# Performance work log

Measured on AMD Instinct MI355X. Metric: run time of the kernel, lower is better.

The kernel has to match this reference:

```python
import jax, jax.numpy as jnp
import numpy as np

N_ATOMS = 100000
N_BONDS = 200000
N_MOLS = 4000
ATOMS_PER_MOL = 25
MAX_NB = 6
ATOM_FDIM = 133
BOND_FDIM = 14
HIDDEN = 300
DEPTH = 3


def setup_inputs() -> dict:
    key = jax.random.key(0)
    ks = jax.random.split(key, 8)
    f_atoms = jax.random.normal(ks[0], (N_ATOMS, ATOM_FDIM), dtype=jnp.float32)
    f_bonds = jax.random.normal(ks[1], (N_BONDS, BOND_FDIM), dtype=jnp.float32)
    # incoming-bond lists per atom (irregular gather targets)
    a2b = jax.random.randint(ks[2], (N_ATOMS, MAX_NB), 0, N_BONDS, dtype=jnp.int32)
    # source atom of each directed bond
    b2a = jax.random.randint(ks[3], (N_BONDS,), 0, N_ATOMS, dtype=jnp.int32)
    # reverse bond: directed bonds come in pairs (2i, 2i+1)
    b2revb = (jnp.arange(N_BONDS, dtype=jnp.int32) ^ 1)
    # contiguous [start, size] per molecule
    starts = jnp.arange(N_MOLS, dtype=jnp.int32) * ATOMS_PER_MOL
    sizes = jnp.full((N_MOLS,), ATOMS_PER_MOL, dtype=jnp.int32)
    a_scope = jnp.stack([starts, sizes], axis=1)
    W_i = jax.random.normal(ks[4], (HIDDEN, ATOM_FDIM + BOND_FDIM), dtype=jnp.float32) * 0.05
    W_h = jax.random.normal(ks[5], (HIDDEN, HIDDEN), dtype=jnp.float32) * 0.05
    W_o = jax.random.normal(ks[6], (HIDDEN, ATOM_FDIM + HIDDEN), dtype=jnp.float32) * 0.05
    b_o = jax.random.normal(ks[7], (HIDDEN,), dtype=jnp.float32) * 0.05
    return {"f_atoms": f_atoms, "f_bonds": f_bonds, "a2b": a2b, "b2a": b2a,
            "b2revb": b2revb, "a_scope": a_scope, "W_i": W_i, "W_h": W_h,
            "W_o": W_o, "b_o": b_o}


def reference(f_atoms, f_bonds, a2b, b2a, b2revb, a_scope, W_i, W_h, W_o, b_o):
    # initial directed-bond messages: [f_atoms[src], f_bonds] -> Linear -> ReLU
    input_feats = jnp.concatenate([f_atoms[b2a], f_bonds], axis=1)  # (E, 147)
    message = jax.nn.relu(input_feats @ W_i.T)  # (E, H)
    for _ in range(DEPTH - 1):
        nei_a_message = message[a2b].sum(axis=1)          # (V, H) gather+sum
        nei_message = nei_a_message[b2a] - message[b2revb]  # (E, H)
        message = jax.nn.relu(nei_message @ W_h.T)
    a_message = message[a2b].sum(axis=1)  # (V, H)
    atom_hiddens = jax.nn.relu(jnp.concatenate([f_atoms, a_message], axis=1) @ W_o.T + b_o)
    # vectorized scope mean-pool (scopes are contiguous ranges)
    starts = a_scope[:, 0]
    sizes = a_scope[:, 1]
    seg_ids = jnp.searchsorted(starts, jnp.arange(atom_hiddens.shape[0]), side='right') - 1
    sums = jax.ops.segment_sum(atom_hiddens, seg_ids, num_segments=N_MOLS)
    denom = jnp.maximum(sizes, 1).astype(atom_hiddens.dtype)[:, None]
    mol_vecs = jnp.where((sizes > 0)[:, None], sums / denom, 0.0)
    return mol_vecs
```

## Files before the change

### kernel.cpp

```cpp
#include <hip/hip_runtime.h>
#include <stdint.h>

#define N_ATOMS   100000
#define N_BONDS   200000
#define N_MOLS    4000
#define MAX_NB    6
#define ATOM_FDIM 133
#define BOND_FDIM 14
#define HIDDEN    300
#define NPAD      320

typedef __attribute__((ext_vector_type(8))) short          bf16x8;
typedef __attribute__((ext_vector_type(8))) unsigned short u16x8;
typedef __attribute__((ext_vector_type(4))) float          f32x4;
typedef __attribute__((ext_vector_type(4))) unsigned int   u32x4;

static __device__ __forceinline__ float u2f(unsigned int u) {
  union { unsigned int u; float f; } v; v.u = u; return v.f;
}
static __device__ __forceinline__ unsigned int f2u(float f) {
  union { float f; unsigned int u; } v; v.f = f; return v.u;
}
static __device__ __forceinline__ float bflo(unsigned int u) { return u2f(u << 16); }
static __device__ __forceinline__ float bfhi(unsigned int u) { return u2f(u & 0xffff0000u); }
static __device__ __forceinline__ unsigned short f2bf_rn(float f) {
  unsigned int u = f2u(f);
  return (unsigned short)((u + 0x7fffu + ((u >> 16) & 1u)) >> 16);
}
static __device__ __forceinline__ unsigned int pack_rn(float lo, float hi) {
  return ((unsigned int)f2bf_rn(hi) << 16) | f2bf_rn(lo);
}

__global__ __launch_bounds__(256) void convw_kernel(
    const float* __restrict__ w, unsigned short* __restrict__ o,
    int Ksrc, int seg1, int src2off, int seg2dst, int seg2len, int KP) {
  int total = NPAD * KP;
  for (int idx = blockIdx.x * 256 + threadIdx.x; idx < total; idx += gridDim.x * 256) {
    int n = idx / KP, k = idx - n * KP;
    int src = -1;
    if (k < seg1) src = k;
    else if (k >= seg2dst && k < seg2dst + seg2len) src = src2off + (k - seg2dst);
    float v = (n < HIDDEN && src >= 0) ? w[(size_t)n * Ksrc + src] : 0.f;
    o[idx] = f2bf_rn(v);
  }
}

template<int KP, int SRC, bool RELU, bool BIAS>
__global__ __launch_bounds__(256, 2) void gemm_bp(
    const float* __restrict__ Af, const float* __restrict__ F2,
    const unsigned short* Ab, const unsigned short* __restrict__ Nei,
    const int* __restrict__ gmap, const unsigned short* __restrict__ W,
    const float* __restrict__ bias, unsigned short* out, int M) {
  constexpr int NST = KP / 32;
  __shared__ __align__(16) unsigned short As[NST * 2048];

  const int b0   = blockIdx.x * 64;
  const int tid  = threadIdx.x;
  const int lane = tid & 63;
  const int wave = tid >> 6;
  const int sr   = tid >> 2;
  const int q    = tid & 3;

  int row = b0 + sr;
  if (row >= M) row = M - 1;
  int g = 0;
  if (SRC == 0 || SRC == 3) g = gmap[row];
  const int rev = row ^ 1;
  const int dbase = (sr >> 4) * 512 + (q * 16 + (sr & 15)) * 8;

  auto stage_chunk = [&](int ks) -> u16x8 {
    const int kc = ks * 32 + q * 8;
    u16x8 r;
    if (SRC == 1) {
      r = *(const u16x8*)(Ab + (size_t)row * KP + kc);
    } else if (SRC == 3) {
      u16x8 n8 = *(const u16x8*)(Nei + (size_t)g * NPAD + kc);
      u16x8 z8 = *(const u16x8*)(Ab + (size_t)rev * NPAD + kc);
#pragma unroll
      for (int j = 0; j < 8; j += 2) {
        unsigned int nu = ((const unsigned int*)&n8)[j >> 1];
        unsigned int zu = ((const unsigned int*)&z8)[j >> 1];
        float lo = bflo(nu) - bflo(zu), hi = bfhi(nu) - bfhi(zu);
        lo = lo > 0.f ? lo : 0.f; hi = hi > 0.f ? hi : 0.f;
        ((unsigned int*)&r)[j >> 1] = pack_rn(lo, hi);
      }
    } else if (SRC == 0) {
#pragma unroll
      for (int j = 0; j < 8; j++) {
        int k = kc + j; float v = 0.f;
        if (k < ATOM_FDIM) v = Af[(size_t)g * ATOM_FDIM + k];
        else if (k >= 160 && k < 160 + BOND_FDIM) v = F2[(size_t)row * BOND_FDIM + (k - 160)];
        r[j] = f2bf_rn(v);
      }
    } else {
      if (kc >= 160) {
        r = *(const u16x8*)(Ab + (size_t)row * NPAD + (kc - 160));
      } else {
#pragma unroll
        for (int j = 0; j < 8; j++) {
          int k = kc + j;
          r[j] = (k < ATOM_FDIM) ? f2bf_rn(Af[(size_t)row * ATOM_FDIM + k]) : (unsigned short)0;
        }
      }
    }
    return r;
  };

  constexpr int G = (NST < 5) ? NST : 5;
#pragma unroll
  for (int ks0 = 0; ks0 < NST; ks0 += G) {
    u16x8 vals[G];
#pragma unroll
    for (int j = 0; j < G; j++) { int ks = ks0 + j; if (ks < NST) vals[j] = stage_chunk(ks); }
#pragma unroll
    for (int j = 0; j < G; j++) { int ks = ks0 + j; if (ks < NST) *(u16x8*)&As[ks * 2048 + dbase] = vals[j]; }
  }
  __syncthreads();

  f32x4 acc[4][5];
#pragma unroll
  for (int m = 0; m < 4; m++)
#pragma unroll
    for (int n = 0; n < 5; n++) acc[m][n] = (f32x4){0.f, 0.f, 0.f, 0.f};

  const int nbase = wave * 80;
  const int ar = lane & 15, kq = lane >> 4;
  const unsigned short* Wl = W + (size_t)(nbase + ar) * KP + kq * 8;

  bf16x8 bnxt[5];
#pragma unroll
  for (int nf = 0; nf < 5; nf++) bnxt[nf] = *(const bf16x8*)(Wl + (size_t)nf * 16 * KP);

#pragma unroll
  for (int ks = 0; ks < NST; ks++) {
    bf16x8 bcur[5];
#pragma unroll
    for (int nf = 0; nf < 5; nf++) bcur[nf] = bnxt[nf];
    if (ks + 1 < NST) {
#pragma unroll
      for (int nf = 0; nf < 5; nf++)
        bnxt[nf] = *(const bf16x8*)(Wl + (size_t)nf * 16 * KP + (ks + 1) * 32);
    }
    bf16x8 af[4];
#pragma unroll
    for (int m = 0; m < 4; m++) af[m] = *(const bf16x8*)&As[ks * 2048 + m * 512 + lane * 8];
#pragma unroll
    for (int nf = 0; nf < 5; nf++)
#pragma unroll
      for (int m = 0; m < 4; m++)
        acc[m][nf] = __builtin_amdgcn_mfma_f32_16x16x32_bf16(af[m], bcur[nf], acc[m][nf], 0, 0, 0);
  }

#pragma unroll
  for (int m = 0; m < 4; m++) {
#pragma unroll
    for (int rr = 0; rr < 4; rr++) {
      int orow = b0 + m * 16 + kq * 4 + rr;
      if (orow >= M) continue;
#pragma unroll
      for (int nf = 0; nf < 5; nf++) {
        int ocol = nbase + nf * 16 + ar;
        float v = acc[m][nf][rr];
        if (BIAS) v += (ocol < HIDDEN) ? bias[ocol] : 0.f;
        if (RELU) v = v > 0.f ? v : 0.f;
        out[(size_t)orow * NPAD + ocol] = f2bf_rn(v);
      }
    }
  }
}

__global__ __launch_bounds__(256) void agg_kernel(
    const unsigned short* __restrict__ src, const int* __restrict__ a2b,
    unsigned short* __restrict__ dst) {
  const int TPA = NPAD / 16;
  int idx = blockIdx.x * 256 + threadIdx.x;
  if (idx >= N_ATOMS * TPA) return;
  int a  = idx / TPA;
  int kc = (idx - a * TPA) * 16;
  int bidx[MAX_NB];
#pragma unroll
  for (int j = 0; j < MAX_NB; j++) bidx[j] = a2b[a * MAX_NB + j];
  float slo[8], shi[8];
#pragma unroll
  for (int t = 0; t < 8; t++) { slo[t] = 0.f; shi[t] = 0.f; }
#pragma unroll
  for (int j = 0; j < MAX_NB; j++) {
    const u32x4* p = (const u32x4*)(src + (size_t)bidx[j] * NPAD + kc);
    u32x4 v0 = p[0], v1 = p[1];
#pragma unroll
    for (int t = 0; t < 4; t++) {
      slo[t]     += bflo(v0[t]); shi[t]     += bfhi(v0[t]);
      slo[4 + t] += bflo(v1[t]); shi[4 + t] += bfhi(v1[t]);
    }
  }
  u32x4 o0, o1;
#pragma unroll
  for (int t = 0; t < 4; t++) { o0[t] = pack_rn(slo[t], shi[t]); o1[t] = pack_rn(slo[4 + t], shi[4 + t]); }
  u32x4* qp = (u32x4*)(dst + (size_t)a * NPAD + kc);
  qp[0] = o0; qp[1] = o1;
}

__global__ __launch_bounds__(256) void combineH_kernel(
    const unsigned short* __restrict__ neiZ, const unsigned short* Zh,
    const int* __restrict__ b2a, unsigned short* msg) {
  const int TPB = NPAD / 16;
  const int NPAIR = N_BONDS / 2;
  int idx = blockIdx.x * 256 + threadIdx.x;
  if (idx >= NPAIR * TPB) return;
  int p  = idx / TPB;
  int kc = (idx - p * TPB) * 16;
  int b0i = 2 * p, b1i = 2 * p + 1;
  int g0 = b2a[b0i], g1 = b2a[b1i];
  const u32x4* pn0 = (const u32x4*)(neiZ + (size_t)g0 * NPAD + kc);
  const u32x4* pn1 = (const u32x4*)(neiZ + (size_t)g1 * NPAD + kc);
  const u32x4* pz0 = (const u32x4*)(Zh + (size_t)b1i * NPAD + kc);
  const u32x4* pz1 = (const u32x4*)(Zh + (size_t)b0i * NPAD + kc);
  u32x4 n00 = pn0[0], n01 = pn0[1], n10 = pn1[0], n11 = pn1[1];
  u32x4 z00 = pz0[0], z01 = pz0[1], z10 = pz1[0], z11 = pz1[1];
  u32x4 o00, o01, o10, o11;
#pragma unroll
  for (int t = 0; t < 4; t++) {
    float a, c;
    a = bflo(n00[t]) - bflo(z00[t]); c = bfhi(n00[t]) - bfhi(z00[t]);
    o00[t] = pack_rn(a > 0.f ? a : 0.f, c > 0.f ? c : 0.f);
    a = bflo(n01[t]) - bflo(z01[t]); c = bfhi(n01[t]) - bfhi(z01[t]);
    o01[t] = pack_rn(a > 0.f ? a : 0.f, c > 0.f ? c : 0.f);
    a = bflo(n10[t]) - bflo(z10[t]); c = bfhi(n10[t]) - bfhi(z10[t]);
    o10[t] = pack_rn(a > 0.f ? a : 0.f, c > 0.f ? c : 0.f);
    a = bflo(n11[t]) - bflo(z11[t]); c = bfhi(n11[t]) - bfhi(z11[t]);
    o11[t] = pack_rn(a > 0.f ? a : 0.f, c > 0.f ? c : 0.f);
  }
  u32x4* q0 = (u32x4*)(msg + (size_t)b0i * NPAD + kc);
  u32x4* q1 = (u32x4*)(msg + (size_t)b1i * NPAD + kc);
  q0[0] = o00; q0[1] = o01; q1[0] = o10; q1[1] = o11;
}

__global__ __launch_bounds__(256) void readout_kernel(
    const unsigned short* __restrict__ hidden, const int* __restrict__ a_scope,
    float* __restrict__ out) {
  const int TPM = NPAD / 8;
  int idx = blockIdx.x * 256 + threadIdx.x;
  if (idx >= N_MOLS * TPM) return;
  int m = idx / TPM;
  int c = (idx - m * TPM) * 8;
  int start = a_scope[m * 2], size = a_scope[m * 2 + 1];
  float s[8];
#pragma unroll
  for (int t = 0; t < 8; t++) s[t] = 0.f;
  for (int i = 0; i < size; i++) {
    const u32x4 v = *(const u32x4*)(hidden + (size_t)(start + i) * NPAD + c);
#pragma unroll
    for (int t = 0; t < 4; t++) { s[2 * t] += bflo(v[t]); s[2 * t + 1] += bfhi(v[t]); }
  }
  float inv = (size > 0) ? 1.f / (float)size : 0.f;
#pragma unroll
  for (int t = 0; t < 8; t++) {
    int col = c + t;
    if (col < HIDDEN) out[(size_t)m * HIDDEN + col] = s[t] * inv;
  }
}

extern "C" void kernel_launch(void* const* d_in, const int* in_sizes, int n_in,
                              void* d_out, int out_size, void* d_ws, size_t ws_size,
                              hipStream_t stream) {
  const float* f_atoms = (const float*)d_in[0];
  const float* f_bonds = (const float*)d_in[1];
  const int*   a2b     = (const int*)d_in[2];
  const int*   b2a     = (const int*)d_in[3];
  const int*   a_scope = (const int*)d_in[5];
  const float* W_i     = (const float*)d_in[6];
  const float* W_h     = (const float*)d_in[7];
  const float* W_o     = (const float*)d_in[8];
  const float* b_o     = (const float*)d_in[9];
  float* out = (float*)d_out;

  char* ws = (char*)d_ws;
  size_t off = 0;
  auto alloc = [&](size_t bytes) { size_t o = off; off += (bytes + 255) & ~(size_t)255; return o; };
  unsigned short* P    = (unsigned short*)(ws + alloc((size_t)N_BONDS * NPAD * 2));
  unsigned short* Q    = (unsigned short*)(ws + alloc((size_t)N_BONDS * NPAD * 2));
  unsigned short* WiAB = (unsigned short*)(ws + alloc((size_t)NPAD * 192 * 2));
  unsigned short* Wh   = (unsigned short*)(ws + alloc((size_t)NPAD * 320 * 2));
  unsigned short* Wo   = (unsigned short*)(ws + alloc((size_t)NPAD * 480 * 2));

  convw_kernel<<<(NPAD * 192 + 255) / 256, 256, 0, stream>>>(W_i, WiAB, 147, 133, 133, 160, 14, 192);
  convw_kernel<<<(NPAD * 320 + 255) / 256, 256, 0, stream>>>(W_h, Wh, 300, 300, 0, 0, 0, 320);
  convw_kernel<<<(NPAD * 480 + 255) / 256, 256, 0, stream>>>(W_o, Wo, 433, 133, 133, 160, 300, 480);

  const int gridB = (N_BONDS + 63) / 64;
  const int gridA = (N_ATOMS + 63) / 64;
  const int gagg = (N_ATOMS * (NPAD / 16) + 255) / 256;
  const int gpar = ((N_BONDS / 2) * (NPAD / 16) + 255) / 256;

  gemm_bp<192, 0, true, false><<<gridB, 256, 0, stream>>>(
      f_atoms, f_bonds, nullptr, nullptr, b2a, WiAB, nullptr, P, N_BONDS);

  gemm_bp<320, 1, false, false><<<gridB, 256, 0, stream>>>(
      nullptr, nullptr, P, nullptr, nullptr, Wh, nullptr, Q, N_BONDS);

  agg_kernel<<<gagg, 256, 0, stream>>>(Q, a2b, P);

  gemm_bp<320, 3, false, false><<<gridB, 256, 0, stream>>>(
      nullptr, nullptr, Q, P, b2a, Wh, nullptr, Q, N_BONDS);

  agg_kernel<<<gagg, 256, 0, stream>>>(Q, a2b, P);
  combineH_kernel<<<gpar, 256, 0, stream>>>(P, Q, b2a, Q);

  agg_kernel<<<gagg, 256, 0, stream>>>(Q, a2b, P);
  gemm_bp<480, 2, true, true><<<gridA, 256, 0, stream>>>(
      f_atoms, nullptr, P, nullptr, nullptr, Wo, b_o, Q, N_ATOMS);

  readout_kernel<<<(N_MOLS * (NPAD / 8) + 255) / 256, 256, 0, stream>>>(Q, a_scope, out);
}
```

Measured before the change: 723.1 us.

## Add persistent double-buffered bond GEMM with async LDS loads and bf16 inputs

Adds a persistent GEMM kernel for the bond-side layers that double-buffers the A tile in LDS using global_load_lds, overlapping the next tile's loads with the current MFMA work. Atom and bond features are pre-converted to padded bf16 so the first layer's gather can be issued as direct 16-byte async loads. The message passing is reorganised to reuse the agg and combineH kernels rather than fusing the subtraction into the GEMM staging. Intermediate buffers are cut to one bond-sized buffer plus an atom-sized one, which adds two conversion passes and an in-place GEMM output.

```diff
diff --git a/kernel.cpp b/kernel.cpp
--- a/kernel.cpp
+++ b/kernel.cpp
@@ -29,6 +29,16 @@
 }
 static __device__ __forceinline__ unsigned int pack_rn(float lo, float hi) {
   return ((unsigned int)f2bf_rn(hi) << 16) | f2bf_rn(lo);
+}
+
+__global__ __launch_bounds__(256) void convin_kernel(
+    const float* __restrict__ w, unsigned short* __restrict__ o, int N, int K, int KP) {
+  size_t total = (size_t)N * KP;
+  for (size_t idx = (size_t)blockIdx.x * 256 + threadIdx.x; idx < total; idx += (size_t)gridDim.x * 256) {
+    int n = (int)(idx / KP), k = (int)(idx - (size_t)n * KP);
+    float v = (k < K) ? w[(size_t)n * K + k] : 0.f;
+    o[idx] = f2bf_rn(v);
+  }
 }
 
 __global__ __launch_bounds__(256) void convw_kernel(
@@ -45,6 +55,110 @@
   }
 }
 
+template<int KP, int SEG, bool RELU>
+__global__ __launch_bounds__(256) void gemm_tp(
+    const unsigned short* S1, const unsigned short* __restrict__ S2,
+    const int* __restrict__ gmap, const unsigned short* __restrict__ W,
+    unsigned short* out, int M, int nTiles) {
+  constexpr int CHUNKS = KP / 8;
+  constexpr int NST    = KP / 32;
+  __shared__ __align__(16) unsigned short As[2 * 64 * KP];
+
+  const int tid  = threadIdx.x;
+  const int lane = tid & 63;
+  const int wv   = tid >> 6;
+  const int ar   = lane & 15, kq = lane >> 4;
+  const int nbase = wv * 80;
+  const unsigned short* Wl = W + (size_t)(nbase + ar) * KP + kq * 8;
+
+  auto rowof = [&](int tile) { int r = tile * 64 + lane; return (r < M) ? r : (M - 1); };
+
+  auto stage = [&](int buf, int drow, int srow) {
+    char* base = (char*)As + (size_t)buf * (64 * KP * 2);
+#pragma unroll
+    for (int cs = wv; cs < CHUNKS; cs += 4) {
+      const unsigned short* src;
+      if (SEG == 0) src = S1 + (size_t)drow * KP + cs * 8;
+      else src = (cs < 20) ? (S1 + (size_t)srow * 160 + cs * 8)
+                           : (S2 + (size_t)drow * 32 + (cs - 20) * 8);
+      __builtin_amdgcn_global_load_lds(
+          (const __attribute__((address_space(1))) void*)src,
+          (__attribute__((address_space(3))) void*)(base + (size_t)cs * 1024), 16, 0, 0);
+    }
+  };
+
+  f32x4 acc[4][5];
+
+  auto compute = [&](int buf) {
+    const char* base = (const char*)As + (size_t)buf * (64 * KP * 2);
+    bf16x8 bnxt[5];
+#pragma unroll
+    for (int nf = 0; nf < 5; nf++) bnxt[nf] = *(const bf16x8*)(Wl + (size_t)nf * 16 * KP);
+#pragma unroll
+    for (int ks = 0; ks < NST; ks++) {
+      bf16x8 bcur[5];
+#pragma unroll
+      for (int nf = 0; nf < 5; nf++) bcur[nf] = bnxt[nf];
+      if (ks + 1 < NST) {
+#pragma unroll
+        for (int nf = 0; nf < 5; nf++)
+          bnxt[nf] = *(const bf16x8*)(Wl + (size_t)nf * 16 * KP + (ks + 1) * 32);
+      }
+      bf16x8 af[4];
+#pragma unroll
+      for (int m = 0; m < 4; m++)
+        af[m] = *(const bf16x8*)(base + (size_t)((ks * 4 + kq) * 64 + m * 16 + ar) * 16);
+#pragma unroll
+      for (int nf = 0; nf < 5; nf++)
+#pragma unroll
+        for (int m = 0; m < 4; m++)
+          acc[m][nf] = __builtin_amdgcn_mfma_f32_16x16x32_bf16(af[m], bcur[nf], acc[m][nf], 0, 0, 0);
+    }
+  };
+
+  auto storeC = [&](int tile) {
+#pragma unroll
+    for (int m = 0; m < 4; m++)
+#pragma unroll
+      for (int rr = 0; rr < 4; rr++) {
+        int orow = tile * 64 + m * 16 + kq * 4 + rr;
+        if (orow >= M) continue;
+#pragma unroll
+        for (int nf = 0; nf < 5; nf++) {
+          float v = acc[m][nf][rr];
+          if (RELU) v = v > 0.f ? v : 0.f;
+          out[(size_t)orow * NPAD + nbase + nf * 16 + ar] = f2bf_rn(v);
+        }
+      }
+  };
+
+  int t = blockIdx.x;
+  if (t >= nTiles) return;
+  {
+    int srow0 = (SEG == 1) ? gmap[rowof(t)] : 0;
+    stage(0, rowof(t), srow0);
+  }
+  int tn = t + gridDim.x;
+  int g_n = (SEG == 1 && tn < nTiles) ? gmap[rowof(tn)] : 0;
+  __syncthreads();
+
+  int cur = 0;
+  while (t < nTiles) {
+    const int nxt = t + gridDim.x;
+    if (nxt < nTiles) stage(cur ^ 1, rowof(nxt), g_n);
+    const int t2 = nxt + gridDim.x;
+    int g_n2 = (SEG == 1 && t2 < nTiles) ? gmap[rowof(t2)] : 0;
+#pragma unroll
+    for (int m = 0; m < 4; m++)
+#pragma unroll
+      for (int n = 0; n < 5; n++) acc[m][n] = (f32x4){0.f, 0.f, 0.f, 0.f};
+    compute(cur);
+    __syncthreads();
+    storeC(t);
+    cur ^= 1; t = nxt; g_n = g_n2;
+  }
+}
+
 template<int KP, int SRC, bool RELU, bool BIAS>
 __global__ __launch_bounds__(256, 2) void gemm_bp(
     const float* __restrict__ Af, const float* __restrict__ F2,
@@ -63,50 +177,24 @@
 
   int row = b0 + sr;
   if (row >= M) row = M - 1;
-  int g = 0;
-  if (SRC == 0 || SRC == 3) g = gmap[row];
-  const int rev = row ^ 1;
   const int dbase = (sr >> 4) * 512 + (q * 16 + (sr & 15)) * 8;
 
   auto stage_chunk = [&](int ks) -> u16x8 {
     const int kc = ks * 32 + q * 8;
     u16x8 r;
-    if (SRC == 1) {
-      r = *(const u16x8*)(Ab + (size_t)row * KP + kc);
-    } else if (SRC == 3) {
-      u16x8 n8 = *(const u16x8*)(Nei + (size_t)g * NPAD + kc);
-      u16x8 z8 = *(const u16x8*)(Ab + (size_t)rev * NPAD + kc);
-#pragma unroll
-      for (int j = 0; j < 8; j += 2) {
-        unsigned int nu = ((const unsigned int*)&n8)[j >> 1];
-        unsigned int zu = ((const unsigned int*)&z8)[j >> 1];
-        float lo = bflo(nu) - bflo(zu), hi = bfhi(nu) - bfhi(zu);
-        lo = lo > 0.f ? lo : 0.f; hi = hi > 0.f ? hi : 0.f;
-        ((unsigned int*)&r)[j >> 1] = pack_rn(lo, hi);
-      }
-    } else if (SRC == 0) {
+    if (kc >= 160) {
+      r = *(const u16x8*)(Ab + (size_t)row * NPAD + (kc - 160));
+    } else {
 #pragma unroll
       for (int j = 0; j < 8; j++) {
-        int k = kc + j; float v = 0.f;
-        if (k < ATOM_FDIM) v = Af[(size_t)g * ATOM_FDIM + k];
-        else if (k >= 160 && k < 160 + BOND_FDIM) v = F2[(size_t)row * BOND_FDIM + (k - 160)];
-        r[j] = f2bf_rn(v);
-      }
-    } else {
-      if (kc >= 160) {
-        r = *(const u16x8*)(Ab + (size_t)row * NPAD + (kc - 160));
-      } else {
-#pragma unroll
-        for (int j = 0; j < 8; j++) {
-          int k = kc + j;
-          r[j] = (k < ATOM_FDIM) ? f2bf_rn(Af[(size_t)row * ATOM_FDIM + k]) : (unsigned short)0;
-        }
+        int k = kc + j;
+        r[j] = (k < ATOM_FDIM) ? f2bf_rn(Af[(size_t)row * ATOM_FDIM + k]) : (unsigned short)0;
       }
     }
     return r;
   };
 
-  constexpr int G = (NST < 5) ? NST : 5;
+  constexpr int G = 5;
 #pragma unroll
   for (int ks0 = 0; ks0 < NST; ks0 += G) {
     u16x8 vals[G];
@@ -277,38 +365,40 @@
   char* ws = (char*)d_ws;
   size_t off = 0;
   auto alloc = [&](size_t bytes) { size_t o = off; off += (bytes + 255) & ~(size_t)255; return o; };
-  unsigned short* P    = (unsigned short*)(ws + alloc((size_t)N_BONDS * NPAD * 2));
-  unsigned short* Q    = (unsigned short*)(ws + alloc((size_t)N_BONDS * NPAD * 2));
-  unsigned short* WiAB = (unsigned short*)(ws + alloc((size_t)NPAD * 192 * 2));
-  unsigned short* Wh   = (unsigned short*)(ws + alloc((size_t)NPAD * 320 * 2));
-  unsigned short* Wo   = (unsigned short*)(ws + alloc((size_t)NPAD * 480 * 2));
-
+  unsigned short* P     = (unsigned short*)(ws + alloc((size_t)N_BONDS * NPAD * 2));
+  unsigned short* R     = (unsigned short*)(ws + alloc((size_t)N_ATOMS * NPAD * 2));
+  unsigned short* fa_bf = (unsigned short*)(ws + alloc((size_t)N_ATOMS * 160 * 2));
+  unsigned short* fb_bf = (unsigned short*)(ws + alloc((size_t)N_BONDS * 32 * 2));
+  unsigned short* WiAB  = (unsigned short*)(ws + alloc((size_t)NPAD * 192 * 2));
+  unsigned short* Wh    = (unsigned short*)(ws + alloc((size_t)NPAD * 320 * 2));
+  unsigned short* Wo    = (unsigned short*)(ws + alloc((size_t)NPAD * 480 * 2));
+
+  convin_kernel<<<2048, 256, 0, stream>>>(f_atoms, fa_bf, N_ATOMS, ATOM_FDIM, 160);
+  convin_kernel<<<2048, 256, 0, stream>>>(f_bonds, fb_bf, N_BONDS, BOND_FDIM, 32);
   convw_kernel<<<(NPAD * 192 + 255) / 256, 256, 0, stream>>>(W_i, WiAB, 147, 133, 133, 160, 14, 192);
   convw_kernel<<<(NPAD * 320 + 255) / 256, 256, 0, stream>>>(W_h, Wh, 300, 300, 0, 0, 0, 320);
   convw_kernel<<<(NPAD * 480 + 255) / 256, 256, 0, stream>>>(W_o, Wo, 433, 133, 133, 160, 300, 480);
 
-  const int gridB = (N_BONDS + 63) / 64;
-  const int gridA = (N_ATOMS + 63) / 64;
+  const int nTilesB = N_BONDS / 64;
   const int gagg = (N_ATOMS * (NPAD / 16) + 255) / 256;
   const int gpar = ((N_BONDS / 2) * (NPAD / 16) + 255) / 256;
-
-  gemm_bp<192, 0, true, false><<<gridB, 256, 0, stream>>>(
-      f_atoms, f_bonds, nullptr, nullptr, b2a, WiAB, nullptr, P, N_BONDS);
-
-  gemm_bp<320, 1, false, false><<<gridB, 256, 0, stream>>>(
-      nullptr, nullptr, P, nullptr, nullptr, Wh, nullptr, Q, N_BONDS);
-
-  agg_kernel<<<gagg, 256, 0, stream>>>(Q, a2b, P);
-
-  gemm_bp<320, 3, false, false><<<gridB, 256, 0, stream>>>(
-      nullptr, nullptr, Q, P, b2a, Wh, nullptr, Q, N_BONDS);
-
-  agg_kernel<<<gagg, 256, 0, stream>>>(Q, a2b, P);
-  combineH_kernel<<<gpar, 256, 0, stream>>>(P, Q, b2a, Q);
-
-  agg_kernel<<<gagg, 256, 0, stream>>>(Q, a2b, P);
+  const int gridA = (N_ATOMS + 63) / 64;
+
+  gemm_tp<192, 1, true><<<768, 256, 0, stream>>>(
+      fa_bf, fb_bf, b2a, WiAB, P, N_BONDS, nTilesB);
+
+  gemm_tp<320, 0, false><<<512, 256, 0, stream>>>(
+      P, nullptr, nullptr, Wh, P, N_BONDS, nTilesB);
+  agg_kernel<<<gagg, 256, 0, stream>>>(P, a2b, R);
+  combineH_kernel<<<gpar, 256, 0, stream>>>(R, P, b2a, P);
+
+  gemm_tp<320, 0, false><<<512, 256, 0, stream>>>(
+      P, nullptr, nullptr, Wh, P, N_BONDS, nTilesB);
+  agg_kernel<<<gagg, 256, 0, stream>>>(P, a2b, R);
+  combineH_kernel<<<gpar, 256, 0, stream>>>(R, P, b2a, P);
+
+  agg_kernel<<<gagg, 256, 0, stream>>>(P, a2b, R);
   gemm_bp<480, 2, true, true><<<gridA, 256, 0, stream>>>(
-      f_atoms, nullptr, P, nullptr, nullptr, Wo, b_o, Q, N_ATOMS);
-
-  readout_kernel<<<(N_MOLS * (NPAD / 8) + 255) / 256, 256, 0, stream>>>(Q, a_scope, out);
-}
+      f_atoms, nullptr, R, nullptr, nullptr, Wo, b_o, R, N_ATOMS);
+  readout_kernel<<<(N_MOLS * (NPAD / 8) + 255) / 256, 256, 0, stream>>>(R, a_scope, out);
+}
```

After: 668.8 us. 1.08x faster.
